# Performance work log

Measured on AMD Instinct MI355X. Metric: run time of the kernel, lower is better.

## Reference

```python
import jax, jax.numpy as jnp
import numpy as np

T, B, IN, H = 256, 64, 512, 1024

def setup_inputs() -> dict:
    key = jax.random.key(0)
    ks = jax.random.split(key, 8)
    s_in = 1.0 / np.sqrt(IN)
    s_h = 1.0 / np.sqrt(H)
    return {
        "inp": jax.random.normal(ks[0], (T, B, IN), jnp.float32),
        "img": jax.random.normal(ks[1], (B, H), jnp.float32),
        "Wxh": jax.random.uniform(ks[2], (4 * H, IN), jnp.float32, -s_in, s_in),
        "bxh": jax.random.uniform(ks[3], (4 * H,), jnp.float32, -s_in, s_in),
        "Whh": jax.random.uniform(ks[4], (4 * H, H), jnp.float32, -s_h, s_h),
        "bhh": jax.random.uniform(ks[5], (4 * H,), jnp.float32, -s_h, s_h),
        "Wout": jax.random.uniform(ks[6], (IN, H), jnp.float32, -s_h, s_h),
        "bout": jax.random.uniform(ks[7], (IN,), jnp.float32, -s_h, s_h),
    }

def reference(inp, img, Wxh, bxh, Whh, bhh, Wout, bout):
    t_len, b, _ = inp.shape
    h_dim = Whh.shape[1]
    img4 = jnp.concatenate([img, img, img, img], axis=1)  # [B, 4H]
    # precompute input projection for all timesteps: [T, B, 4H]
    xproj = jnp.einsum('tbi,gi->tbg', inp, Wxh) + bxh
    xproj = xproj.at[0].add(img4)

    def step(carry, xg):
        h, c = carry
        gates = xg + h @ Whh.T + bhh  # [B, 4H]
        i_g, f_g, g_g, o_g = jnp.split(gates, 4, axis=1)
        c = jax.nn.sigmoid(f_g) * c + jax.nn.sigmoid(i_g) * jnp.tanh(g_g)
        h = jax.nn.sigmoid(o_g) * jnp.tanh(c)
        return (h, c), h

    zeros = jnp.zeros((b, h_dim), inp.dtype)
    _, hs = jax.lax.scan(step, (zeros, zeros), xproj)  # hs: [T, B, H]
    out = jnp.einsum('tbh,vh->tbv', hs, Wout) + bout  # [T, B, IN]
    return jax.nn.log_softmax(out, axis=-1)
```

## Files before the change

### kernel.cpp

```cpp
#include <hip/hip_runtime.h>
#include <math.h>

#define T_LEN 256
#define B_SZ  64
#define IN_D  512
#define H_D   1024
#define G4    4096

typedef float  f32x4 __attribute__((ext_vector_type(4)));
typedef short  s16x8 __attribute__((ext_vector_type(8)));
typedef unsigned int u32x4 __attribute__((ext_vector_type(4)));
typedef unsigned short u16;
typedef unsigned int   u32;

__device__ __forceinline__ void gl_lds16(const void* g, void* l) {
  __builtin_amdgcn_global_load_lds(
      (const __attribute__((address_space(1))) unsigned int*)g,
      (__attribute__((address_space(3))) unsigned int*)l, 16, 0, 0);
}

__device__ __forceinline__ u16 f2bf(float f) {
  union { float f; unsigned u; } v; v.f = f;
  unsigned x = v.u;
  unsigned r = (x + 0x7fffu + ((x >> 16) & 1u)) >> 16;
  return (u16)r;
}
__device__ __forceinline__ float bf2f(u16 b) {
  union { unsigned u; float f; } v; v.u = ((unsigned)b) << 16;
  return v.f;
}
__device__ __forceinline__ float sigm(float x) {
  return 1.0f / (1.0f + __expf(-x));
}
__device__ __forceinline__ float tanh_f(float x) {
  float e = __expf(2.0f * x);
  return 1.0f - 2.0f / (e + 1.0f);
}

__global__ void cvt_f32_bf16(const float* __restrict__ src, u16* __restrict__ dst, int n) {
  int i = blockIdx.x * blockDim.x + threadIdx.x;
  int stride = gridDim.x * blockDim.x;
  for (; i < n; i += stride) dst[i] = f2bf(src[i]);
}

__global__ void fill_sentinel(u32* __restrict__ p, int n4) {
  int i = blockIdx.x * blockDim.x + threadIdx.x;
  int stride = gridDim.x * blockDim.x;
  u32x4 s = {0xFFFFFFFFu, 0xFFFFFFFFu, 0xFFFFFFFFu, 0xFFFFFFFFu};
  for (; i < n4; i += stride) {
    u32* dst = p + (size_t)i * 4;
    asm volatile("global_store_dwordx4 %0, %1, off sc1" :: "v"(dst), "v"(s) : "memory");
  }
}

template<int KD, int EPI>
__launch_bounds__(256)
__global__ void gemm_bt(const u16* __restrict__ A, const u16* __restrict__ Bm,
                        const float* __restrict__ bias, const float* __restrict__ img,
                        u16* __restrict__ Cb, float* __restrict__ Cf, int Ncols) {
  __shared__ u16 sA[128 * 64];
  __shared__ u16 sB[128 * 64];
  const int tid  = threadIdx.x;
  const int wave = tid >> 6, lane = tid & 63;
  const int wm = wave >> 1, wn = wave & 1;
  const int mBase = blockIdx.y * 128;
  const int nBase = blockIdx.x * 128;

  f32x4 acc[4][4] = {};

  for (int k0 = 0; k0 < KD; k0 += 64) {
#pragma unroll
    for (int it = 0; it < 4; ++it) {
      int s = it * 256 + tid;
      int row = s >> 3, c = s & 7;
      int gc = c ^ (row & 7);
      const u16* ga = A  + (size_t)(mBase + row) * KD + k0 + gc * 8;
      const u16* gb = Bm + (size_t)(nBase + row) * KD + k0 + gc * 8;
      gl_lds16(ga, &sA[(it * 256 + wave * 64) * 8]);
      gl_lds16(gb, &sB[(it * 256 + wave * 64) * 8]);
    }
    __syncthreads();

    const int q = lane >> 4, rl = lane & 15;
#pragma unroll
    for (int ks = 0; ks < 64; ks += 32) {
      s16x8 af[4], bfr[4];
      int gcb = (ks >> 3) + q;
#pragma unroll
      for (int i = 0; i < 4; ++i) {
        int rowA = wm * 64 + i * 16 + rl;
        af[i]  = *(const s16x8*)&sA[rowA * 64 + (gcb ^ (rowA & 7)) * 8];
        int rowB = wn * 64 + i * 16 + rl;
        bfr[i] = *(const s16x8*)&sB[rowB * 64 + (gcb ^ (rowB & 7)) * 8];
      }
#pragma unroll
      for (int i = 0; i < 4; ++i)
#pragma unroll
        for (int j = 0; j < 4; ++j)
          acc[i][j] = __builtin_amdgcn_mfma_f32_16x16x32_bf16(af[i], bfr[j], acc[i][j], 0, 0, 0);
    }
    __syncthreads();
  }

#pragma unroll
  for (int i = 0; i < 4; ++i) {
    int rbase = mBase + wm * 64 + i * 16 + ((lane >> 4) << 2);
#pragma unroll
    for (int j = 0; j < 4; ++j) {
      int col = nBase + wn * 64 + j * 16 + (lane & 15);
      float bc = bias[col];
#pragma unroll
      for (int r = 0; r < 4; ++r) {
        int row = rbase + r;
        float v = acc[i][j][r] + bc;
        if (EPI == 0) {
          if (row < B_SZ) v += img[row * H_D + (col & (H_D - 1))];
          Cb[(size_t)row * Ncols + col] = f2bf(v);
        } else {
          Cf[(size_t)row * Ncols + col] = v;
        }
      }
    }
  }
}

__launch_bounds__(256, 1)
__global__ void lstm_rec(const u16* __restrict__ WhhB, const u16* __restrict__ xproj,
                         const float* __restrict__ bhh, u32* __restrict__ hs32) {
  __shared__ u16  sH[16 * 1024];
  __shared__ float sGp[16][16][17];

  const int tid  = threadIdx.x;
  const int wave = tid >> 6, lane = tid & 63;
  const int grp = blockIdx.x >> 6;
  const int wg  = blockIdx.x & 63;
  const int bBase = grp * 16;
  const int colBase = wg * 16;
  const int q = lane >> 4, rl = lane & 15;

  s16x8 wf[4][8];
  {
    const u16* wb = WhhB + (size_t)(colBase + rl) * H_D + wave * 256 + q * 8;
#pragma unroll
    for (int g = 0; g < 4; ++g)
#pragma unroll
      for (int m = 0; m < 8; ++m)
        wf[g][m] = *(const s16x8*)(wb + (size_t)g * H_D * H_D + m * 32);
  }

  float cst = 0.f;
  const int ub = tid >> 4, uc = tid & 15;
  const int gb = bBase + ub;
  const int gcol = colBase + uc;
  const float bh_i = bhh[0 * H_D + gcol], bh_f = bhh[1 * H_D + gcol];
  const float bh_g = bhh[2 * H_D + gcol], bh_o = bhh[3 * H_D + gcol];

  for (int t = 0; t < T_LEN; ++t) {
    const u16* xp = xproj + ((size_t)t * B_SZ + gb) * G4;
    float gi_ = bf2f(xp[0 * H_D + gcol]) + bh_i;
    float gf_ = bf2f(xp[1 * H_D + gcol]) + bh_f;
    float gg_ = bf2f(xp[2 * H_D + gcol]) + bh_g;
    float go_ = bf2f(xp[3 * H_D + gcol]) + bh_o;

    if (t > 0) {
      u32x4 v[8];
      const u32* hp = hs32 + (size_t)(t - 1) * B_SZ * 512 + (size_t)bBase * 512;
#pragma unroll
      for (int j = 0; j < 8; ++j) {
        int cid = j * 256 + tid;
        const u32* p = hp + (cid >> 7) * 512 + (cid & 127) * 4;
        asm volatile("global_load_dwordx4 %0, %1, off sc1"
                     : "=v"(v[j]) : "v"(p) : "memory");
      }
      asm volatile("s_waitcnt vmcnt(0)" ::: "memory");
      for (;;) {
        u32 bad = 0;
#pragma unroll
        for (int j = 0; j < 8; ++j) {
          bool st = (v[j][0] == 0xFFFFFFFFu) | (v[j][1] == 0xFFFFFFFFu) |
                    (v[j][2] == 0xFFFFFFFFu) | (v[j][3] == 0xFFFFFFFFu);
          bad |= st ? (1u << j) : 0u;
        }
        if (!bad) break;
#pragma unroll
        for (int j = 0; j < 8; ++j) {
          if (bad & (1u << j)) {
            int cid = j * 256 + tid;
            const u32* p = hp + (cid >> 7) * 512 + (cid & 127) * 4;
            asm volatile("global_load_dwordx4 %0, %1, off sc1"
                         : "=v"(v[j]) : "v"(p) : "memory");
          }
        }
        asm volatile("s_waitcnt vmcnt(0)" ::: "memory");
      }
#pragma unroll
      for (int j = 0; j < 8; ++j) {
        int cid = j * 256 + tid;
        int r = cid >> 7, c = cid & 127;
        *(s16x8*)&sH[r * 1024 + (c ^ (r & 7)) * 8] = *(s16x8*)&v[j];
      }
      __syncthreads();

      f32x4 a0 = {}, a1 = {}, a2 = {}, a3 = {};
#pragma unroll
      for (int m = 0; m < 8; ++m) {
        int chunk = wave * 32 + m * 4 + q;
        s16x8 afr = *(const s16x8*)&sH[rl * 1024 + ((chunk ^ (rl & 7))) * 8];
        a0 = __builtin_amdgcn_mfma_f32_16x16x32_bf16(afr, wf[0][m], a0, 0, 0, 0);
        a1 = __builtin_amdgcn_mfma_f32_16x16x32_bf16(afr, wf[1][m], a1, 0, 0, 0);
        a2 = __builtin_amdgcn_mfma_f32_16x16x32_bf16(afr, wf[2][m], a2, 0, 0, 0);
        a3 = __builtin_amdgcn_mfma_f32_16x16x32_bf16(afr, wf[3][m], a3, 0, 0, 0);
      }
#pragma unroll
      for (int r = 0; r < 4; ++r) {
        int row = (lane >> 4) * 4 + r;
        sGp[wave * 4 + 0][row][lane & 15] = a0[r];
        sGp[wave * 4 + 1][row][lane & 15] = a1[r];
        sGp[wave * 4 + 2][row][lane & 15] = a2[r];
        sGp[wave * 4 + 3][row][lane & 15] = a3[r];
      }
      __syncthreads();
      gi_ += sGp[0][ub][uc] + sGp[4][ub][uc] + sGp[8][ub][uc]  + sGp[12][ub][uc];
      gf_ += sGp[1][ub][uc] + sGp[5][ub][uc] + sGp[9][ub][uc]  + sGp[13][ub][uc];
      gg_ += sGp[2][ub][uc] + sGp[6][ub][uc] + sGp[10][ub][uc] + sGp[14][ub][uc];
      go_ += sGp[3][ub][uc] + sGp[7][ub][uc] + sGp[11][ub][uc] + sGp[15][ub][uc];
    }

    cst = sigm(gf_) * cst + sigm(gi_) * tanh_f(gg_);
    float h = sigm(go_) * tanh_f(cst);

    u32 b = f2bf(h);
    u32 p1 = (u32)__shfl_xor((int)b, 1);
    u32 w0 = b | (p1 << 16);
    u32 w1 = (u32)__shfl_xor((int)w0, 2);
    u32 w2 = (u32)__shfl_xor((int)w0, 4);
    u32 w3 = (u32)__shfl_xor((int)w1, 4);
    if ((tid & 7) == 0) {
      u32x4 pk = {w0, w1, w2, w3};
      u32* dst = hs32 + ((size_t)t * B_SZ + gb) * 512 + (gcol >> 1);
      asm volatile("global_store_dwordx4 %0, %1, off sc1"
                   :: "v"(dst), "v"(pk) : "memory");
    }
  }
  asm volatile("s_waitcnt vmcnt(0)" ::: "memory");
}

__launch_bounds__(256)
__global__ void logsoftmax_rows(float* __restrict__ out) {
  __shared__ float red[8];
  float* p = out + (size_t)blockIdx.x * IN_D;
  const int tid = threadIdx.x;
  float v0 = p[tid], v1 = p[tid + 256];
  float m = fmaxf(v0, v1);
#pragma unroll
  for (int off = 32; off > 0; off >>= 1) m = fmaxf(m, __shfl_down(m, off));
  if ((tid & 63) == 0) red[tid >> 6] = m;
  __syncthreads();
  m = fmaxf(fmaxf(red[0], red[1]), fmaxf(red[2], red[3]));
  float e = __expf(v0 - m) + __expf(v1 - m);
#pragma unroll
  for (int off = 32; off > 0; off >>= 1) e += __shfl_down(e, off);
  if ((tid & 63) == 0) red[4 + (tid >> 6)] = e;
  __syncthreads();
  float ls = m + logf(red[4] + red[5] + red[6] + red[7]);
  p[tid] = v0 - ls;
  p[tid + 256] = v1 - ls;
}

extern "C" void kernel_launch(void* const* d_in, const int* in_sizes, int n_in,
                              void* d_out, int out_size, void* d_ws, size_t ws_size,
                              hipStream_t stream) {
  const float* inp  = (const float*)d_in[0];
  const float* img  = (const float*)d_in[1];
  const float* Wxh  = (const float*)d_in[2];
  const float* bxh  = (const float*)d_in[3];
  const float* Whh  = (const float*)d_in[4];
  const float* bhh  = (const float*)d_in[5];
  const float* Wout = (const float*)d_in[6];
  const float* bout = (const float*)d_in[7];
  float* out = (float*)d_out;

  char* ws = (char*)d_ws;
  u16* inpB   = (u16*)(ws);
  u16* WxhB   = (u16*)(ws + 16777216);
  u16* WhhB   = (u16*)(ws + 20971520);
  u16* WoutB  = (u16*)(ws + 29360128);
  u16* xprojB = (u16*)(ws + 30408704);
  u16* hsB    = (u16*)(ws + 164626432);

  fill_sentinel<<<2048, 256, 0, stream>>>((u32*)hsB, T_LEN * B_SZ * 512 / 4);

  cvt_f32_bf16<<<2048, 256, 0, stream>>>(inp,  inpB,  T_LEN * B_SZ * IN_D);
  cvt_f32_bf16<<<2048, 256, 0, stream>>>(Wxh,  WxhB,  G4 * IN_D);
  cvt_f32_bf16<<<2048, 256, 0, stream>>>(Whh,  WhhB,  G4 * H_D);
  cvt_f32_bf16<<<2048, 256, 0, stream>>>(Wout, WoutB, IN_D * H_D);

  gemm_bt<IN_D, 0><<<dim3(G4 / 128, 16384 / 128), 256, 0, stream>>>(
      inpB, WxhB, bxh, img, xprojB, nullptr, G4);

  lstm_rec<<<256, 256, 0, stream>>>(WhhB, xprojB, bhh, (u32*)hsB);

  gemm_bt<H_D, 1><<<dim3(IN_D / 128, 16384 / 128), 256, 0, stream>>>(
      hsB, WoutB, bout, nullptr, nullptr, out, IN_D);

  logsoftmax_rows<<<16384, 256, 0, stream>>>(out);
}
```

Measured before the change: 1.022 ms.

## Load h fragments directly into MFMA registers and double-buffer gate partials

Each lane now loads the previous-step hidden-state fragment it needs straight from global memory into registers in MFMA operand layout. This removes the LDS staging buffer for h and one __syncthreads per timestep. The gate partial-sum buffer is double-buffered by timestep parity, so the remaining single barrier is enough to avoid write-after-read races. The spin-wait exit is now decided per wave with __any, and sched_barriers keep the loads ordered.

```diff
diff --git a/kernel.cpp b/kernel.cpp
--- a/kernel.cpp
+++ b/kernel.cpp
@@ -127,8 +127,7 @@
 __launch_bounds__(256, 1)
 __global__ void lstm_rec(const u16* __restrict__ WhhB, const u16* __restrict__ xproj,
                          const float* __restrict__ bhh, u32* __restrict__ hs32) {
-  __shared__ u16  sH[16 * 1024];
-  __shared__ float sGp[16][16][17];
+  __shared__ float sGp[2][16][16][17];
 
   const int tid  = threadIdx.x;
   const int wave = tid >> 6, lane = tid & 63;
@@ -164,66 +163,55 @@
 
     if (t > 0) {
       u32x4 v[8];
-      const u32* hp = hs32 + (size_t)(t - 1) * B_SZ * 512 + (size_t)bBase * 512;
-#pragma unroll
-      for (int j = 0; j < 8; ++j) {
-        int cid = j * 256 + tid;
-        const u32* p = hp + (cid >> 7) * 512 + (cid & 127) * 4;
+      const u32* hp = hs32 + (size_t)(t - 1) * B_SZ * 512 + (size_t)bBase * 512
+                    + rl * 512 + wave * 128 + q * 4;
+#pragma unroll
+      for (int m = 0; m < 8; ++m)
         asm volatile("global_load_dwordx4 %0, %1, off sc1"
-                     : "=v"(v[j]) : "v"(p) : "memory");
-      }
+                     : "=v"(v[m]) : "v"(hp + m * 16) : "memory");
       asm volatile("s_waitcnt vmcnt(0)" ::: "memory");
+      __builtin_amdgcn_sched_barrier(0);
       for (;;) {
         u32 bad = 0;
 #pragma unroll
-        for (int j = 0; j < 8; ++j) {
-          bool st = (v[j][0] == 0xFFFFFFFFu) | (v[j][1] == 0xFFFFFFFFu) |
-                    (v[j][2] == 0xFFFFFFFFu) | (v[j][3] == 0xFFFFFFFFu);
-          bad |= st ? (1u << j) : 0u;
+        for (int m = 0; m < 8; ++m) {
+          bool st = (v[m][0] == 0xFFFFFFFFu) | (v[m][1] == 0xFFFFFFFFu) |
+                    (v[m][2] == 0xFFFFFFFFu) | (v[m][3] == 0xFFFFFFFFu);
+          bad |= st ? (1u << m) : 0u;
         }
-        if (!bad) break;
-#pragma unroll
-        for (int j = 0; j < 8; ++j) {
-          if (bad & (1u << j)) {
-            int cid = j * 256 + tid;
-            const u32* p = hp + (cid >> 7) * 512 + (cid & 127) * 4;
+        if (!__any((int)bad)) break;
+#pragma unroll
+        for (int m = 0; m < 8; ++m)
+          if (bad & (1u << m))
             asm volatile("global_load_dwordx4 %0, %1, off sc1"
-                         : "=v"(v[j]) : "v"(p) : "memory");
-          }
-        }
+                         : "=v"(v[m]) : "v"(hp + m * 16) : "memory");
         asm volatile("s_waitcnt vmcnt(0)" ::: "memory");
-      }
-#pragma unroll
-      for (int j = 0; j < 8; ++j) {
-        int cid = j * 256 + tid;
-        int r = cid >> 7, c = cid & 127;
-        *(s16x8*)&sH[r * 1024 + (c ^ (r & 7)) * 8] = *(s16x8*)&v[j];
-      }
-      __syncthreads();
+        __builtin_amdgcn_sched_barrier(0);
+      }
 
       f32x4 a0 = {}, a1 = {}, a2 = {}, a3 = {};
 #pragma unroll
       for (int m = 0; m < 8; ++m) {
-        int chunk = wave * 32 + m * 4 + q;
-        s16x8 afr = *(const s16x8*)&sH[rl * 1024 + ((chunk ^ (rl & 7))) * 8];
+        s16x8 afr = *(const s16x8*)&v[m];
         a0 = __builtin_amdgcn_mfma_f32_16x16x32_bf16(afr, wf[0][m], a0, 0, 0, 0);
         a1 = __builtin_amdgcn_mfma_f32_16x16x32_bf16(afr, wf[1][m], a1, 0, 0, 0);
         a2 = __builtin_amdgcn_mfma_f32_16x16x32_bf16(afr, wf[2][m], a2, 0, 0, 0);
         a3 = __builtin_amdgcn_mfma_f32_16x16x32_bf16(afr, wf[3][m], a3, 0, 0, 0);
       }
+      const int p = t & 1;
 #pragma unroll
       for (int r = 0; r < 4; ++r) {
         int row = (lane >> 4) * 4 + r;
-        sGp[wave * 4 + 0][row][lane & 15] = a0[r];
-        sGp[wave * 4 + 1][row][lane & 15] = a1[r];
-        sGp[wave * 4 + 2][row][lane & 15] = a2[r];
-        sGp[wave * 4 + 3][row][lane & 15] = a3[r];
+        sGp[p][wave * 4 + 0][row][lane & 15] = a0[r];
+        sGp[p][wave * 4 + 1][row][lane & 15] = a1[r];
+        sGp[p][wave * 4 + 2][row][lane & 15] = a2[r];
+        sGp[p][wave * 4 + 3][row][lane & 15] = a3[r];
       }
       __syncthreads();
-      gi_ += sGp[0][ub][uc] + sGp[4][ub][uc] + sGp[8][ub][uc]  + sGp[12][ub][uc];
-      gf_ += sGp[1][ub][uc] + sGp[5][ub][uc] + sGp[9][ub][uc]  + sGp[13][ub][uc];
-      gg_ += sGp[2][ub][uc] + sGp[6][ub][uc] + sGp[10][ub][uc] + sGp[14][ub][uc];
-      go_ += sGp[3][ub][uc] + sGp[7][ub][uc] + sGp[11][ub][uc] + sGp[15][ub][uc];
+      gi_ += sGp[p][0][ub][uc] + sGp[p][4][ub][uc] + sGp[p][8][ub][uc]  + sGp[p][12][ub][uc];
+      gf_ += sGp[p][1][ub][uc] + sGp[p][5][ub][uc] + sGp[p][9][ub][uc]  + sGp[p][13][ub][uc];
+      gg_ += sGp[p][2][ub][uc] + sGp[p][6][ub][uc] + sGp[p][10][ub][uc] + sGp[p][14][ub][uc];
+      go_ += sGp[p][3][ub][uc] + sGp[p][7][ub][uc] + sGp[p][11][ub][uc] + sGp[p][15][ub][uc];
     }
 
     cst = sigm(gf_) * cst + sigm(gi_) * tanh_f(gg_);
```

Result: slower. 1.087 ms (+6.3%).
